# Kernel optimization log

Measured on AMD Instinct MI355X. Metric: run time of the kernel, lower is better.

## Reference

```python
import jax, jax.numpy as jnp
import numpy as np

B_SZ, L, H, P = 16, 1024, 256, 256
DT_MIN, DT_MAX = 1e-3, 1e-1


def setup_inputs() -> dict:
    key = jax.random.key(0)
    ks = jax.random.split(key, 6)
    u = jax.random.normal(ks[0], (B_SZ, L, H), dtype=jnp.float32)
    # Stable diagonal init (stands in for HiPPO-LegS diag: negative real part,
    # spread imaginary parts) so exp(Lambda*Delta) has |.|<1 over long scans.
    Lambda_re = -0.5 * jnp.ones((P,), jnp.float32)
    Lambda_im = jnp.pi * jnp.arange(P, dtype=jnp.float32)
    Bp = jax.random.normal(ks[1], (P, H, 2), jnp.float32) / jnp.sqrt(2.0 * H)  # (P,H,2) real/imag
    Cp = jax.random.normal(ks[2], (H, P, 2), jnp.float32) / jnp.sqrt(2.0 * P)  # (H,P,2) real/imag
    D = jax.random.normal(ks[3], (H,), jnp.float32)
    log_step = (jax.random.uniform(ks[4], (P, 1), jnp.float32)
                * (jnp.log(DT_MAX) - jnp.log(DT_MIN)) + jnp.log(DT_MIN))
    return {"u": u, "Lambda_re": Lambda_re, "Lambda_im": Lambda_im,
            "B": Bp, "C": Cp, "D": D, "log_step": log_step}


def _binop(ei, ej):
    # S5 associative scan element: (A, Bu); compose linear recurrences.
    ai, bi = ei
    aj, bj = ej
    return aj * ai, aj * bi + bj


def reference(u, Lambda_re, Lambda_im, B, C, D, log_step):
    # clip_eigs=False, step_rescale=1.0, conj_sym=True, discretization='zoh'
    Lambda = Lambda_re + 1j * Lambda_im                     # (P,) complex
    B_tilde = B[..., 0] + 1j * B[..., 1]                    # (P,H) complex
    C_tilde = C[..., 0] + 1j * C[..., 1]                    # (H,P) complex
    Delta = jnp.exp(log_step[:, 0])                         # (P,)
    # ZOH discretization
    Lambda_bar = jnp.exp(Lambda * Delta)                    # (P,)
    B_bar = ((Lambda_bar - 1.0) / Lambda)[:, None] * B_tilde  # (P,H)
    # Input projection: (B, L, P) complex
    Bu = jnp.einsum('ph,blh->blp', B_bar, u.astype(B_bar.dtype))
    Lam = jnp.broadcast_to(Lambda_bar, Bu.shape)            # (B, L, P)
    # Parallel associative scan over time axis
    _, xs = jax.lax.associative_scan(_binop, (Lam, Bu), axis=1)  # states (B,L,P)
    # Output projection; conj_sym -> 2 * real part
    ys = 2.0 * jnp.einsum('hp,blp->blh', C_tilde, xs).real  # (B,L,H)
    return ys + D * u                                       # feedthrough
```

## Files before the change

kernel.cpp:

```cpp
#include <hip/hip_runtime.h>
#include <hip/hip_bf16.h>
#include <math.h>

#define BB     16
#define LSEQ   1024
#define HH     256
#define PP     256
#define MROWS  (BB*LSEQ)
#define LC     32
#define NC     (LSEQ/LC)
#define NCHUNK (BB*NC)

#define OFF_W1T  0u
#define OFF_W2T  262144u
#define OFF_PW   524288u
#define OFF_CEND 655360u
#define OFF_CARR 1703936u
#define OFF_XS   2752512u

#define XSTRIDE 520

typedef __attribute__((ext_vector_type(8))) short short8;
typedef __attribute__((ext_vector_type(4))) float floatx4;

__device__ __forceinline__ float bf2f(unsigned hs) {
    union { unsigned u; float f; } v; v.u = hs << 16; return v.f;
}
__device__ __forceinline__ unsigned short f2bs(float f) {
    __hip_bfloat16 h = __float2bfloat16(f);
    union { __hip_bfloat16 h; unsigned short s; } v; v.h = h; return v.s;
}
__device__ __forceinline__ unsigned packbf(float r, float i) {
    return (unsigned)f2bs(r) | ((unsigned)f2bs(i) << 16);
}
__device__ __forceinline__ void async16(const void* g, void* l) {
    __builtin_amdgcn_global_load_lds(
        (const __attribute__((address_space(1))) unsigned*)g,
        (__attribute__((address_space(3))) unsigned*)l, 16, 0, 0);
}
__device__ __forceinline__ float2 lam_pow(float lr, float li, float dtt) {
    float m = expf(lr * dtt);
    return make_float2(m * cosf(li * dtt), m * sinf(li * dtt));
}

__global__ void k_prep(const float* __restrict__ Bm, const float* __restrict__ Cm,
                       const float* __restrict__ Lr, const float* __restrict__ Li,
                       const float* __restrict__ ls, char* __restrict__ ws) {
    int blk = blockIdx.x, t = threadIdx.x;
    if (blk < 256) {
        int p = blk, h = t;
        float lr = Lr[p], li = Li[p];
        float dt = expf(ls[p]);
        float2 lam = lam_pow(lr, li, dt);
        float den = lr * lr + li * li;
        float nr = lam.x - 1.0f, ni = lam.y;
        float cr = (nr * lr + ni * li) / den;
        float ci = (ni * lr - nr * li) / den;
        float br = Bm[(p * HH + h) * 2 + 0];
        float bi = Bm[(p * HH + h) * 2 + 1];
        unsigned short* w1 = (unsigned short*)(ws + OFF_W1T);
        w1[(2 * p) * 256 + h]     = f2bs(cr * br - ci * bi);
        w1[(2 * p + 1) * 256 + h] = f2bs(cr * bi + ci * br);
        if (t <= 32)
            ((float2*)(ws + OFF_PW))[t * 256 + p] = lam_pow(lr, li, dt * (float)t);
    } else {
        int h = blk - 256, p = t;
        float c_r = Cm[(h * PP + p) * 2 + 0];
        float c_i = Cm[(h * PP + p) * 2 + 1];
        ((unsigned*)(ws + OFF_W2T))[h * 256 + p] = packbf(2.0f * c_r, -2.0f * c_i);
    }
}

__global__ __launch_bounds__(512, 2) void k_g1scan(
        const float* __restrict__ u, const float* __restrict__ Lr,
        const float* __restrict__ Li, const float* __restrict__ ls,
        char* __restrict__ ws) {
    __shared__ char smem[4096 + 65536];
    char* Asb = smem;
    char* Bsb = smem + 4096;
    unsigned short* X = (unsigned short*)smem;
    unsigned* X32 = (unsigned*)smem;
    const unsigned short* W1 = (const unsigned short*)(ws + OFF_W1T);
    const int tid = threadIdx.x, bc = blockIdx.x;
    const int wave = tid >> 6, lane = tid & 63;
    const int q = lane >> 4, rr = lane & 15;
    const int c4 = lane & 3, r4 = lane >> 2;
    const int m0 = bc * LC;

    floatx4 acc[2][4];
    #pragma unroll
    for (int i = 0; i < 2; ++i)
        #pragma unroll
        for (int j = 0; j < 4; ++j) acc[i][j] = (floatx4)0.0f;

    const int arow = tid >> 4, acol4 = (tid & 15) * 4;
    const int apan = acol4 >> 5, acin = acol4 & 31;
    for (int k0 = 0; k0 < 256; k0 += 64) {
        __syncthreads();
        float4 v = *(const float4*)(u + (size_t)(m0 + arow) * 256 + k0 + acol4);
        *(uint2*)(Asb + apan * 2048 + arow * 64 + acin * 2) =
            make_uint2(packbf(v.x, v.y), packbf(v.z, v.w));
        #pragma unroll
        for (int t = 0; t < 8; ++t) {
            int idx = t * 8 + wave;
            int pan = idx & 1, rowg = idx >> 1;
            int row = rowg * 16 + r4;
            async16(W1 + (size_t)row * 256 + k0 + pan * 32 + c4 * 8,
                    Bsb + pan * 32768 + row * 64 + c4 * 16);
        }
        __syncthreads();
        #pragma unroll
        for (int ks = 0; ks < 2; ++ks) {
            short8 a0 = *(const short8*)(Asb + ks * 2048 + rr * 64 + q * 16);
            short8 a1 = *(const short8*)(Asb + ks * 2048 + (16 + rr) * 64 + q * 16);
            #pragma unroll
            for (int j = 0; j < 4; ++j) {
                short8 b = *(const short8*)(Bsb + ks * 32768 +
                                            ((wave * 4 + j) * 16 + rr) * 64 + q * 16);
                acc[0][j] = __builtin_amdgcn_mfma_f32_16x16x32_bf16(a0, b, acc[0][j], 0, 0, 0);
                acc[1][j] = __builtin_amdgcn_mfma_f32_16x16x32_bf16(a1, b, acc[1][j], 0, 0, 0);
            }
        }
    }
    __syncthreads();
    #pragma unroll
    for (int i = 0; i < 2; ++i)
        #pragma unroll
        for (int j = 0; j < 4; ++j)
            #pragma unroll
            for (int r0 = 0; r0 < 4; ++r0)
                X[(i * 16 + q * 4 + r0) * XSTRIDE + wave * 64 + j * 16 + rr] =
                    f2bs(acc[i][j][r0]);
    __syncthreads();

    if (tid < 256) {
        const int p = tid;
        const float2 lam = lam_pow(Lr[p], Li[p], expf(ls[p]));
        unsigned* xs32 = (unsigned*)(ws + OFF_XS);
        float xr = 0.0f, xi = 0.0f;
        for (int j = 0; j < LC; ++j) {
            unsigned cv = X32[j * (XSTRIDE / 2) + p];
            float br = bf2f(cv & 0xffffu), bi = bf2f(cv >> 16);
            float nr = fmaf(lam.x, xr, fmaf(-lam.y, xi, br));
            float ni = fmaf(lam.x, xi, fmaf(lam.y, xr, bi));
            xr = nr; xi = ni;
            xs32[(size_t)(m0 + j) * 256 + p] = packbf(xr, xi);
        }
        ((float2*)(ws + OFF_CEND))[bc * 256 + p] = make_float2(xr, xi);
    }
}

__global__ void k_carry(const float* __restrict__ Lr, const float* __restrict__ Li,
                        const float* __restrict__ ls, char* __restrict__ ws) {
    int p = threadIdx.x, b = blockIdx.x;
    float dt = expf(ls[p]);
    float2 g = lam_pow(Lr[p], Li[p], dt * (float)LC);
    const float2* cend = (const float2*)(ws + OFF_CEND);
    float2* carr = (float2*)(ws + OFF_CARR);
    float sr = 0.0f, si = 0.0f;
    for (int c = 0; c < NC; ++c) {
        size_t off = (size_t)(b * NC + c) * 256 + p;
        carr[off] = make_float2(sr, si);
        float2 e = cend[off];
        float nr = fmaf(g.x, sr, fmaf(-g.y, si, e.x));
        float ni = fmaf(g.x, si, fmaf(g.y, sr, e.y));
        sr = nr; si = ni;
    }
}

__global__ __launch_bounds__(256, 4) void k_gemm2fix(
        const char* __restrict__ ws_c, const float* __restrict__ D,
        const float* __restrict__ u, float* __restrict__ out) {
    __shared__ char Asb[8192];
    __shared__ char Bsb[16384];
    __shared__ float2 carrs[2][256];
    const unsigned short* W2 = (const unsigned short*)(ws_c + OFF_W2T);
    const unsigned* xs32 = (const unsigned*)(ws_c + OFF_XS);
    const float2* pw = (const float2*)(ws_c + OFF_PW);
    const float2* carr = (const float2*)(ws_c + OFF_CARR);

    const int tid = threadIdx.x;
    const int wave = tid >> 6, lane = tid & 63;
    const int q = lane >> 4, rr = lane & 15;
    const int c4 = lane & 3, r4 = lane >> 2;
    const int wm = wave & 1, wn = wave >> 1;
    const int m0 = blockIdx.y * 64, n0 = blockIdx.x * 128;

    {
        int cbase = m0 >> 5;
        carrs[0][tid] = carr[(size_t)cbase * 256 + tid];
        carrs[1][tid] = carr[(size_t)(cbase + 1) * 256 + tid];
    }

    floatx4 acc[2][4];
    #pragma unroll
    for (int i = 0; i < 2; ++i)
        #pragma unroll
        for (int j = 0; j < 4; ++j) acc[i][j] = (floatx4)0.0f;

    const int row = tid >> 2, qd = tid & 3;
    const int grow = m0 + row;
    const int jj = (grow & (LC - 1)) + 1;
    const int half = row >> 5;

    for (int k0 = 0; k0 < 512; k0 += 64) {
        __syncthreads();
        {
            int p0 = (k0 >> 1) + qd * 8;
            uint4 xa = *(const uint4*)(xs32 + (size_t)grow * 256 + p0);
            uint4 xb = *(const uint4*)(xs32 + (size_t)grow * 256 + p0 + 4);
            unsigned xv[8] = {xa.x, xa.y, xa.z, xa.w, xb.x, xb.y, xb.z, xb.w};
            const float2* pwp = pw + (size_t)jj * 256 + p0;
            const float2* cap = &carrs[half][p0];
            unsigned o[8];
            #pragma unroll
            for (int e = 0; e < 8; ++e) {
                float2 pwv = pwp[e];
                float2 cav = cap[e];
                float fr = pwv.x * cav.x - pwv.y * cav.y;
                float fi = pwv.x * cav.y + pwv.y * cav.x;
                o[e] = packbf(bf2f(xv[e] & 0xffffu) + fr, bf2f(xv[e] >> 16) + fi);
            }
            char* dst = Asb + (qd >> 1) * 4096 + row * 64 + (qd & 1) * 32;
            *(uint4*)dst        = make_uint4(o[0], o[1], o[2], o[3]);
            *(uint4*)(dst + 16) = make_uint4(o[4], o[5], o[6], o[7]);
        }
        #pragma unroll
        for (int t = 0; t < 4; ++t) {
            int idx = t * 4 + wave;
            int pan = idx & 1, rowg = idx >> 1;
            int rw = rowg * 16 + r4;
            async16(W2 + (size_t)(n0 + rw) * 512 + k0 + pan * 32 + c4 * 8,
                    Bsb + pan * 8192 + rw * 64 + c4 * 16);
        }
        __syncthreads();
        #pragma unroll
        for (int ks = 0; ks < 2; ++ks) {
            short8 a[2], bfr[4];
            #pragma unroll
            for (int i = 0; i < 2; ++i)
                a[i] = *(const short8*)(Asb + ks * 4096 +
                                        (wm * 32 + i * 16 + rr) * 64 + q * 16);
            #pragma unroll
            for (int j = 0; j < 4; ++j)
                bfr[j] = *(const short8*)(Bsb + ks * 8192 +
                                          ((wn * 64 + j * 16 + rr)) * 64 + q * 16);
            #pragma unroll
            for (int i = 0; i < 2; ++i)
                #pragma unroll
                for (int j = 0; j < 4; ++j)
                    acc[i][j] = __builtin_amdgcn_mfma_f32_16x16x32_bf16(a[i], bfr[j], acc[i][j], 0, 0, 0);
        }
    }

    #pragma unroll
    for (int i = 0; i < 2; ++i) {
        int mbase = m0 + wm * 32 + i * 16 + q * 4;
        #pragma unroll
        for (int j = 0; j < 4; ++j) {
            int col = n0 + wn * 64 + j * 16 + rr;
            #pragma unroll
            for (int r0 = 0; r0 < 4; ++r0) {
                int rw = mbase + r0;
                size_t gi = (size_t)rw * 256 + col;
                out[gi] = acc[i][j][r0] + D[col] * u[gi];
            }
        }
    }
}

extern "C" void kernel_launch(void* const* d_in, const int* in_sizes, int n_in,
                              void* d_out, int out_size, void* d_ws, size_t ws_size,
                              hipStream_t stream) {
    const float* u  = (const float*)d_in[0];
    const float* Lr = (const float*)d_in[1];
    const float* Li = (const float*)d_in[2];
    const float* Bm = (const float*)d_in[3];
    const float* Cm = (const float*)d_in[4];
    const float* D  = (const float*)d_in[5];
    const float* ls = (const float*)d_in[6];
    float* out = (float*)d_out;
    char* ws = (char*)d_ws;

    k_prep<<<512, 256, 0, stream>>>(Bm, Cm, Lr, Li, ls, ws);
    k_g1scan<<<NCHUNK, 512, 0, stream>>>(u, Lr, Li, ls, ws);
    k_carry<<<BB, 256, 0, stream>>>(Lr, Li, ls, ws);
    k_gemm2fix<<<dim3(2, MROWS / 64), 256, 0, stream>>>(ws, D, u, out);
}
```

Measured before the change: 115.0 us.

## Pre-convert u to bf16 and retile input GEMM+scan into 128x128 blocks

The prep kernel now also converts u to bf16 into the workspace. The first GEMM+chunk-scan kernel switches from 32-row x 512-col tiles (512 blocks) to 128x128 tiles (4 column slices per 128-row group, 512 blocks). Both operands are loaded with async global-to-LDS copies, and the scan runs four 32-step chunks per block over 64 complex states. This cuts the redundant reloading of the full W1 matrix per 32-row chunk and shrinks shared memory, at the cost of an extra pass writing and reading a bf16 copy of u.

```diff
diff --git a/kernel.cpp b/kernel.cpp
--- a/kernel.cpp
+++ b/kernel.cpp
@@ -17,8 +17,7 @@
 #define OFF_CEND 655360u
 #define OFF_CARR 1703936u
 #define OFF_XS   2752512u
-
-#define XSTRIDE 520
+#define OFF_UB   19529728u
 
 typedef __attribute__((ext_vector_type(8))) short short8;
 typedef __attribute__((ext_vector_type(4))) float floatx4;
@@ -45,7 +44,8 @@
 
 __global__ void k_prep(const float* __restrict__ Bm, const float* __restrict__ Cm,
                        const float* __restrict__ Lr, const float* __restrict__ Li,
-                       const float* __restrict__ ls, char* __restrict__ ws) {
+                       const float* __restrict__ ls, const float* __restrict__ u,
+                       char* __restrict__ ws) {
     int blk = blockIdx.x, t = threadIdx.x;
     if (blk < 256) {
         int p = blk, h = t;
@@ -69,84 +69,84 @@
         float c_i = Cm[(h * PP + p) * 2 + 1];
         ((unsigned*)(ws + OFF_W2T))[h * 256 + p] = packbf(2.0f * c_r, -2.0f * c_i);
     }
-}
-
+    uint2* ub = (uint2*)(ws + OFF_UB);
+    const float4* u4 = (const float4*)u;
+    #pragma unroll
+    for (int i = 0; i < 8; ++i) {
+        size_t idx = (size_t)blk * 2048 + i * 256 + t;
+        float4 v = u4[idx];
+        ub[idx] = make_uint2(packbf(v.x, v.y), packbf(v.z, v.w));
+    }
+}
+
+#define XSTR 140
 __global__ __launch_bounds__(512, 2) void k_g1scan(
-        const float* __restrict__ u, const float* __restrict__ Lr,
-        const float* __restrict__ Li, const float* __restrict__ ls,
-        char* __restrict__ ws) {
-    __shared__ char smem[4096 + 65536];
+        const float* __restrict__ Lr, const float* __restrict__ Li,
+        const float* __restrict__ ls, char* __restrict__ ws) {
+    __shared__ char smem[36864];
     char* Asb = smem;
-    char* Bsb = smem + 4096;
+    char* Bsb = smem + 16384;
     unsigned short* X = (unsigned short*)smem;
     unsigned* X32 = (unsigned*)smem;
     const unsigned short* W1 = (const unsigned short*)(ws + OFF_W1T);
-    const int tid = threadIdx.x, bc = blockIdx.x;
+    const unsigned short* UB = (const unsigned short*)(ws + OFF_UB);
+    const int tid = threadIdx.x, bx = blockIdx.x;
+    const int ns = bx & 3, rg = bx >> 2;
+    const int m0 = rg * 128, n0 = ns * 128;
     const int wave = tid >> 6, lane = tid & 63;
     const int q = lane >> 4, rr = lane & 15;
     const int c4 = lane & 3, r4 = lane >> 2;
-    const int m0 = bc * LC;
-
-    floatx4 acc[2][4];
-    #pragma unroll
-    for (int i = 0; i < 2; ++i)
-        #pragma unroll
-        for (int j = 0; j < 4; ++j) acc[i][j] = (floatx4)0.0f;
-
-    const int arow = tid >> 4, acol4 = (tid & 15) * 4;
-    const int apan = acol4 >> 5, acin = acol4 & 31;
+
+    floatx4 acc[8];
+    #pragma unroll
+    for (int i = 0; i < 8; ++i) acc[i] = (floatx4)0.0f;
+
     for (int k0 = 0; k0 < 256; k0 += 64) {
         __syncthreads();
-        float4 v = *(const float4*)(u + (size_t)(m0 + arow) * 256 + k0 + acol4);
-        *(uint2*)(Asb + apan * 2048 + arow * 64 + acin * 2) =
-            make_uint2(packbf(v.x, v.y), packbf(v.z, v.w));
-        #pragma unroll
-        for (int t = 0; t < 8; ++t) {
+        #pragma unroll
+        for (int t = 0; t < 2; ++t) {
             int idx = t * 8 + wave;
             int pan = idx & 1, rowg = idx >> 1;
             int row = rowg * 16 + r4;
-            async16(W1 + (size_t)row * 256 + k0 + pan * 32 + c4 * 8,
-                    Bsb + pan * 32768 + row * 64 + c4 * 16);
+            async16(UB + (size_t)(m0 + row) * 256 + k0 + pan * 32 + c4 * 8,
+                    Asb + pan * 8192 + row * 64 + c4 * 16);
+            async16(W1 + (size_t)(n0 + row) * 256 + k0 + pan * 32 + c4 * 8,
+                    Bsb + pan * 8192 + row * 64 + c4 * 16);
         }
         __syncthreads();
         #pragma unroll
         for (int ks = 0; ks < 2; ++ks) {
-            short8 a0 = *(const short8*)(Asb + ks * 2048 + rr * 64 + q * 16);
-            short8 a1 = *(const short8*)(Asb + ks * 2048 + (16 + rr) * 64 + q * 16);
-            #pragma unroll
-            for (int j = 0; j < 4; ++j) {
-                short8 b = *(const short8*)(Bsb + ks * 32768 +
-                                            ((wave * 4 + j) * 16 + rr) * 64 + q * 16);
-                acc[0][j] = __builtin_amdgcn_mfma_f32_16x16x32_bf16(a0, b, acc[0][j], 0, 0, 0);
-                acc[1][j] = __builtin_amdgcn_mfma_f32_16x16x32_bf16(a1, b, acc[1][j], 0, 0, 0);
+            short8 b = *(const short8*)(Bsb + ks * 8192 + (wave * 16 + rr) * 64 + q * 16);
+            #pragma unroll
+            for (int i = 0; i < 8; ++i) {
+                short8 a = *(const short8*)(Asb + ks * 8192 + (i * 16 + rr) * 64 + q * 16);
+                acc[i] = __builtin_amdgcn_mfma_f32_16x16x32_bf16(a, b, acc[i], 0, 0, 0);
             }
         }
     }
     __syncthreads();
     #pragma unroll
-    for (int i = 0; i < 2; ++i)
-        #pragma unroll
-        for (int j = 0; j < 4; ++j)
-            #pragma unroll
-            for (int r0 = 0; r0 < 4; ++r0)
-                X[(i * 16 + q * 4 + r0) * XSTRIDE + wave * 64 + j * 16 + rr] =
-                    f2bs(acc[i][j][r0]);
+    for (int i = 0; i < 8; ++i)
+        #pragma unroll
+        for (int r0 = 0; r0 < 4; ++r0)
+            X[(i * 16 + q * 4 + r0) * XSTR + wave * 16 + rr] = f2bs(acc[i][r0]);
     __syncthreads();
 
     if (tid < 256) {
-        const int p = tid;
-        const float2 lam = lam_pow(Lr[p], Li[p], expf(ls[p]));
+        const int ch = tid >> 6, pq = tid & 63;
+        const int gp = (n0 >> 1) + pq;
+        const float2 lam = lam_pow(Lr[gp], Li[gp], expf(ls[gp]));
         unsigned* xs32 = (unsigned*)(ws + OFF_XS);
         float xr = 0.0f, xi = 0.0f;
         for (int j = 0; j < LC; ++j) {
-            unsigned cv = X32[j * (XSTRIDE / 2) + p];
+            unsigned cv = X32[(ch * 32 + j) * (XSTR / 2) + pq];
             float br = bf2f(cv & 0xffffu), bi = bf2f(cv >> 16);
             float nr = fmaf(lam.x, xr, fmaf(-lam.y, xi, br));
             float ni = fmaf(lam.x, xi, fmaf(lam.y, xr, bi));
             xr = nr; xi = ni;
-            xs32[(size_t)(m0 + j) * 256 + p] = packbf(xr, xi);
-        }
-        ((float2*)(ws + OFF_CEND))[bc * 256 + p] = make_float2(xr, xi);
+            xs32[(size_t)(m0 + ch * 32 + j) * 256 + gp] = packbf(xr, xi);
+        }
+        ((float2*)(ws + OFF_CEND))[(size_t)(rg * 4 + ch) * 256 + gp] = make_float2(xr, xi);
     }
 }
 
@@ -282,8 +282,8 @@
     float* out = (float*)d_out;
     char* ws = (char*)d_ws;
 
-    k_prep<<<512, 256, 0, stream>>>(Bm, Cm, Lr, Li, ls, ws);
-    k_g1scan<<<NCHUNK, 512, 0, stream>>>(u, Lr, Li, ls, ws);
+    k_prep<<<512, 256, 0, stream>>>(Bm, Cm, Lr, Li, ls, u, ws);
+    k_g1scan<<<512, 512, 0, stream>>>(Lr, Li, ls, ws);
     k_carry<<<BB, 256, 0, stream>>>(Lr, Li, ls, ws);
     k_gemm2fix<<<dim3(2, MROWS / 64), 256, 0, stream>>>(ws, D, u, out);
 }
```

New measurement: 116.5 us. Within noise of the previous version (+1.4%).

## Split first GEMM+scan over column halves and fold carry kernel into second GEMM

Applied to the files above, without the earlier changes.

The first GEMM+scan kernel now gives each chunk two blocks, each covering half of the N dimension. This halves the per-block LDS and accumulators, allowing higher occupancy and twice as many blocks. The separate k_carry launch is removed: each second-GEMM block recomputes its chunk carry-in by summing earlier chunk end states weighted by powers of lambda^LC. That drops one serial kernel and its launch, but adds redundant per-block work (up to 31 loads and FMAs per state) and redoes the u tile conversion in both half-blocks.

```diff
diff --git a/kernel.cpp b/kernel.cpp
--- a/kernel.cpp
+++ b/kernel.cpp
@@ -15,10 +15,7 @@
 #define OFF_W2T  262144u
 #define OFF_PW   524288u
 #define OFF_CEND 655360u
-#define OFF_CARR 1703936u
 #define OFF_XS   2752512u
-
-#define XSTRIDE 520
 
 typedef __attribute__((ext_vector_type(8))) short short8;
 typedef __attribute__((ext_vector_type(4))) float floatx4;
@@ -71,42 +68,45 @@
     }
 }
 
-__global__ __launch_bounds__(512, 2) void k_g1scan(
+#define XSTR2 268
+__global__ __launch_bounds__(512, 6) void k_g1scan(
         const float* __restrict__ u, const float* __restrict__ Lr,
         const float* __restrict__ Li, const float* __restrict__ ls,
         char* __restrict__ ws) {
-    __shared__ char smem[4096 + 65536];
+    __shared__ char smem[36864];
     char* Asb = smem;
     char* Bsb = smem + 4096;
     unsigned short* X = (unsigned short*)smem;
     unsigned* X32 = (unsigned*)smem;
     const unsigned short* W1 = (const unsigned short*)(ws + OFF_W1T);
-    const int tid = threadIdx.x, bc = blockIdx.x;
+    const int tid = threadIdx.x, bx = blockIdx.x;
+    const int nh = bx & 1, bc = bx >> 1;
+    const int m0 = bc * LC, n0 = nh * 256;
     const int wave = tid >> 6, lane = tid & 63;
     const int q = lane >> 4, rr = lane & 15;
     const int c4 = lane & 3, r4 = lane >> 2;
-    const int m0 = bc * LC;
-
-    floatx4 acc[2][4];
+
+    floatx4 acc[2][2];
     #pragma unroll
     for (int i = 0; i < 2; ++i)
         #pragma unroll
-        for (int j = 0; j < 4; ++j) acc[i][j] = (floatx4)0.0f;
+        for (int j = 0; j < 2; ++j) acc[i][j] = (floatx4)0.0f;
 
     const int arow = tid >> 4, acol4 = (tid & 15) * 4;
-    const int apan = acol4 >> 5, acin = acol4 & 31;
     for (int k0 = 0; k0 < 256; k0 += 64) {
         __syncthreads();
-        float4 v = *(const float4*)(u + (size_t)(m0 + arow) * 256 + k0 + acol4);
-        *(uint2*)(Asb + apan * 2048 + arow * 64 + acin * 2) =
-            make_uint2(packbf(v.x, v.y), packbf(v.z, v.w));
-        #pragma unroll
-        for (int t = 0; t < 8; ++t) {
+        {
+            float4 v = *(const float4*)(u + (size_t)(m0 + arow) * 256 + k0 + acol4);
+            *(uint2*)(Asb + (acol4 >> 5) * 2048 + arow * 64 + (acol4 & 31) * 2) =
+                make_uint2(packbf(v.x, v.y), packbf(v.z, v.w));
+        }
+        #pragma unroll
+        for (int t = 0; t < 4; ++t) {
             int idx = t * 8 + wave;
             int pan = idx & 1, rowg = idx >> 1;
             int row = rowg * 16 + r4;
-            async16(W1 + (size_t)row * 256 + k0 + pan * 32 + c4 * 8,
-                    Bsb + pan * 32768 + row * 64 + c4 * 16);
+            async16(W1 + (size_t)(n0 + row) * 256 + k0 + pan * 32 + c4 * 8,
+                    Bsb + pan * 16384 + row * 64 + c4 * 16);
         }
         __syncthreads();
         #pragma unroll
@@ -114,9 +114,9 @@
             short8 a0 = *(const short8*)(Asb + ks * 2048 + rr * 64 + q * 16);
             short8 a1 = *(const short8*)(Asb + ks * 2048 + (16 + rr) * 64 + q * 16);
             #pragma unroll
-            for (int j = 0; j < 4; ++j) {
-                short8 b = *(const short8*)(Bsb + ks * 32768 +
-                                            ((wave * 4 + j) * 16 + rr) * 64 + q * 16);
+            for (int j = 0; j < 2; ++j) {
+                short8 b = *(const short8*)(Bsb + ks * 16384 +
+                                            (wave * 32 + j * 16 + rr) * 64 + q * 16);
                 acc[0][j] = __builtin_amdgcn_mfma_f32_16x16x32_bf16(a0, b, acc[0][j], 0, 0, 0);
                 acc[1][j] = __builtin_amdgcn_mfma_f32_16x16x32_bf16(a1, b, acc[1][j], 0, 0, 0);
             }
@@ -126,58 +126,43 @@
     #pragma unroll
     for (int i = 0; i < 2; ++i)
         #pragma unroll
-        for (int j = 0; j < 4; ++j)
+        for (int j = 0; j < 2; ++j)
             #pragma unroll
             for (int r0 = 0; r0 < 4; ++r0)
-                X[(i * 16 + q * 4 + r0) * XSTRIDE + wave * 64 + j * 16 + rr] =
+                X[(i * 16 + q * 4 + r0) * XSTR2 + wave * 32 + j * 16 + rr] =
                     f2bs(acc[i][j][r0]);
     __syncthreads();
 
-    if (tid < 256) {
-        const int p = tid;
-        const float2 lam = lam_pow(Lr[p], Li[p], expf(ls[p]));
+    if (tid < 128) {
+        const int pq = tid;
+        const int gp = nh * 128 + pq;
+        const float2 lam = lam_pow(Lr[gp], Li[gp], expf(ls[gp]));
         unsigned* xs32 = (unsigned*)(ws + OFF_XS);
         float xr = 0.0f, xi = 0.0f;
         for (int j = 0; j < LC; ++j) {
-            unsigned cv = X32[j * (XSTRIDE / 2) + p];
+            unsigned cv = X32[j * (XSTR2 / 2) + pq];
             float br = bf2f(cv & 0xffffu), bi = bf2f(cv >> 16);
             float nr = fmaf(lam.x, xr, fmaf(-lam.y, xi, br));
             float ni = fmaf(lam.x, xi, fmaf(lam.y, xr, bi));
             xr = nr; xi = ni;
-            xs32[(size_t)(m0 + j) * 256 + p] = packbf(xr, xi);
-        }
-        ((float2*)(ws + OFF_CEND))[bc * 256 + p] = make_float2(xr, xi);
-    }
-}
-
-__global__ void k_carry(const float* __restrict__ Lr, const float* __restrict__ Li,
-                        const float* __restrict__ ls, char* __restrict__ ws) {
-    int p = threadIdx.x, b = blockIdx.x;
-    float dt = expf(ls[p]);
-    float2 g = lam_pow(Lr[p], Li[p], dt * (float)LC);
-    const float2* cend = (const float2*)(ws + OFF_CEND);
-    float2* carr = (float2*)(ws + OFF_CARR);
-    float sr = 0.0f, si = 0.0f;
-    for (int c = 0; c < NC; ++c) {
-        size_t off = (size_t)(b * NC + c) * 256 + p;
-        carr[off] = make_float2(sr, si);
-        float2 e = cend[off];
-        float nr = fmaf(g.x, sr, fmaf(-g.y, si, e.x));
-        float ni = fmaf(g.x, si, fmaf(g.y, sr, e.y));
-        sr = nr; si = ni;
+            xs32[(size_t)(m0 + j) * 256 + gp] = packbf(xr, xi);
+        }
+        ((float2*)(ws + OFF_CEND))[(size_t)bc * 256 + gp] = make_float2(xr, xi);
     }
 }
 
 __global__ __launch_bounds__(256, 4) void k_gemm2fix(
         const char* __restrict__ ws_c, const float* __restrict__ D,
-        const float* __restrict__ u, float* __restrict__ out) {
+        const float* __restrict__ u, float* __restrict__ out,
+        const float* __restrict__ Lr, const float* __restrict__ Li,
+        const float* __restrict__ ls) {
     __shared__ char Asb[8192];
     __shared__ char Bsb[16384];
     __shared__ float2 carrs[2][256];
     const unsigned short* W2 = (const unsigned short*)(ws_c + OFF_W2T);
     const unsigned* xs32 = (const unsigned*)(ws_c + OFF_XS);
     const float2* pw = (const float2*)(ws_c + OFF_PW);
-    const float2* carr = (const float2*)(ws_c + OFF_CARR);
+    const float2* cend = (const float2*)(ws_c + OFF_CEND);
 
     const int tid = threadIdx.x;
     const int wave = tid >> 6, lane = tid & 63;
@@ -187,9 +172,23 @@
     const int m0 = blockIdx.y * 64, n0 = blockIdx.x * 128;
 
     {
-        int cbase = m0 >> 5;
-        carrs[0][tid] = carr[(size_t)cbase * 256 + tid];
-        carrs[1][tid] = carr[(size_t)(cbase + 1) * 256 + tid];
+        const int cbase = m0 >> 5;
+        const int b = cbase >> 5, c = cbase & 31;
+        const int p = tid;
+        const float2 g = lam_pow(Lr[p], Li[p], expf(ls[p]) * (float)LC);
+        float sr = 0.0f, si = 0.0f;
+        float gpr = 1.0f, gpi = 0.0f;
+        for (int k = 0; k < c; ++k) {
+            float2 e = cend[(size_t)(b * NC + (c - 1 - k)) * 256 + p];
+            sr = fmaf(gpr, e.x, fmaf(-gpi, e.y, sr));
+            si = fmaf(gpr, e.y, fmaf(gpi, e.x, si));
+            float t = gpr * g.x - gpi * g.y;
+            gpi = gpr * g.y + gpi * g.x; gpr = t;
+        }
+        carrs[0][p] = make_float2(sr, si);
+        float2 e = cend[(size_t)cbase * 256 + p];
+        carrs[1][p] = make_float2(fmaf(g.x, sr, fmaf(-g.y, si, e.x)),
+                                  fmaf(g.x, si, fmaf(g.y, sr, e.y)));
     }
 
     floatx4 acc[2][4];
@@ -283,7 +282,6 @@
     char* ws = (char*)d_ws;
 
     k_prep<<<512, 256, 0, stream>>>(Bm, Cm, Lr, Li, ls, ws);
-    k_g1scan<<<NCHUNK, 512, 0, stream>>>(u, Lr, Li, ls, ws);
-    k_carry<<<BB, 256, 0, stream>>>(Lr, Li, ls, ws);
-    k_gemm2fix<<<dim3(2, MROWS / 64), 256, 0, stream>>>(ws, D, u, out);
-}
+    k_g1scan<<<1024, 512, 0, stream>>>(u, Lr, Li, ls, ws);
+    k_gemm2fix<<<dim3(2, MROWS / 64), 256, 0, stream>>>(ws, D, u, out, Lr, Li, ls);
+}
```

Result: no change. 113.8 us (median of 2 runs) (-1.0%).
